# Kernel tuning notes

Hardware: AMD Instinct MI355X
Metric: run time of the kernel (lower is better)

## Reference

```python
import jax, jax.numpy as jnp
import numpy as np

L, B, T, H = 2, 512, 4096, 3


def _gru_layer(x, h0, Wih, Whh, bih, bhh):
    # x: [B,T,H], h0: [B,H], Wih/Whh: [3H,H], bih/bhh: [3H]
    gi = jnp.einsum('bth,gh->btg', x, Wih) + bih  # [B,T,3H] input projections

    def step(h, gi_t):
        gh = h @ Whh.T + bhh                      # [B,3H]
        i_r, i_z, i_n = jnp.split(gi_t, 3, axis=-1)
        h_r, h_z, h_n = jnp.split(gh, 3, axis=-1)
        r = jax.nn.sigmoid(i_r + h_r)
        z = jax.nn.sigmoid(i_z + h_z)
        n = jnp.tanh(i_n + r * h_n)
        h_new = (1.0 - z) * n + z * h
        return h_new, h_new

    h_last, ys = jax.lax.scan(step, h0, jnp.swapaxes(gi, 0, 1))  # ys: [T,B,H]
    return jnp.swapaxes(ys, 0, 1), h_last


def setup_inputs() -> dict:
    key = jax.random.key(0)
    ks = jax.random.split(key, 7)
    s = 0.3  # roughly torch's uniform(-1/sqrt(H), 1/sqrt(H)) scale
    return {
        'x': jax.random.normal(ks[0], (B, T, H), jnp.float32),
        'h': jnp.zeros((L, B, H), jnp.float32),
        'W_ih': jax.random.normal(ks[1], (L, 3 * H, H), jnp.float32) * s,
        'W_hh': jax.random.normal(ks[2], (L, 3 * H, H), jnp.float32) * s,
        'b_ih': jax.random.normal(ks[3], (L, 3 * H), jnp.float32) * s,
        'b_hh': jax.random.normal(ks[4], (L, 3 * H), jnp.float32) * s,
        'W_dec': jax.random.normal(ks[5], (1, H), jnp.float32) * s,
        'b_dec': jax.random.normal(ks[6], (1,), jnp.float32) * s,
    }


def reference(x, h, W_ih, W_hh, b_ih, b_hh, W_dec, b_dec):
    hs = []
    out = x
    for l in range(L):  # small fixed layer count
        out, h_l = _gru_layer(out, h[l], W_ih[l], W_hh[l], b_ih[l], b_hh[l])
        hs.append(h_l)
    h_out = jnp.stack(hs, axis=0)          # [L,B,H]
    y = out @ W_dec.T + b_dec              # [B,T,1]
    return (y, h_out)
```

## Files before the change

kernel.cpp:

```cpp
#include <hip/hip_runtime.h>


constexpr int T = 4096;
constexpr int B = 512;
constexpr float LOG2E = 1.44269504088896340736f;

typedef float v2f __attribute__((ext_vector_type(2)));

__device__ __forceinline__ float fexp2(float v) { return __builtin_amdgcn_exp2f(v); }
__device__ __forceinline__ float frcp(float v)  { return __builtin_amdgcn_rcpf(v); }
__device__ __forceinline__ v2f vfma(v2f a, v2f b, v2f c) {
    return __builtin_elementwise_fma(a, b, c);
}
__device__ __forceinline__ v2f sp(float x) { v2f r; r.x = x; r.y = x; return r; }

template<int CTRL>
__device__ __forceinline__ float dppf(float v) {
    return __int_as_float(
        __builtin_amdgcn_update_dpp(0, __float_as_int(v), CTRL, 0xF, 0xF, true));
}

#define GRU_IT(MODE, X0, X1, X2, YV) do {                                      \
    float hb0 = dppf<0x00>(h), hb1 = dppf<0x55>(h), hb2 = dppf<0xAA>(h);       \
    float s0 = dppf<0x114>(hb0), s1 = dppf<0x114>(hb1), s2 = dppf<0x114>(hb2); \
    float in0 = is_q0 ? (X0) : s0;                                             \
    float in1 = is_q0 ? (X1) : s1;                                             \
    float in2 = is_q0 ? (X2) : s2;                                             \
    v2f arz = vfma(wirz0, sp(in0), brz);                  \
    arz = vfma(wirz1, sp(in1), arz);                                           \
    arz = vfma(wirz2, sp(in2), arz);                                           \
    v2f hrz = vfma(whrz1, sp(hb1), whrz0 * sp(hb0));      \
    hrz = vfma(whrz2, sp(hb2), hrz);                                           \
    v2f crz = arz + hrz;                                                       \
    float r  = frcp(1.0f + fexp2(crz.x));                                      \
    float zz = frcp(1.0f + fexp2(crz.y));                                      \
    v2f cnd = vfma(wnd1, sp(hb1), vfma(wnd0, sp(hb0), bnd));    \
    cnd = vfma(wnd2, sp(hb2), cnd);                                            \
    YV = cnd.y;                                                                \
    float gi = fmaf(win1, in1, fmaf(win0, in0, bni));                          \
    gi = fmaf(win2, in2, gi);                                                  \
    float nn = fmaf(-2.0f, frcp(1.0f + fexp2(fmaf(r, cnd.x, gi))), 1.0f);      \
    float omz = 1.0f - zz;                                                     \
    float zh  = zz * h;                                                        \
    float hn  = fmaf(omz, nn, zh);                          \
    if ((MODE) == 0)      h = hn;                                              \
    else if ((MODE) == 1) h = is_q0 ? hn : h;                                  \
    else                  h = is_q0 ? h : hn;                                  \
} while (0)

__global__ __launch_bounds__(64, 1)
void gru_pipe(const float* __restrict__ x,
              const float* __restrict__ h0,
              const float* __restrict__ Wih,
              const float* __restrict__ Whh,
              const float* __restrict__ bih,
              const float* __restrict__ bhh,
              const float* __restrict__ Wdec,
              const float* __restrict__ bdec,
              float* __restrict__ out)
{
    const int lane  = threadIdx.x;
    const int g8    = lane & 7;
    const int layer = (g8 >> 2) & 1;
    const int jj    = g8 & 3;
    const int j     = jj > 2 ? 2 : jj;
    const bool dummy = (jj == 3);
    const bool is_q0 = (layer == 0);
    const int b = (blockIdx.x * 64 + lane) >> 3;

    const float zm = dummy ? 0.0f : 1.0f;
    const float sR = -LOG2E * zm, sN = 2.0f * LOG2E * zm;
    const float* Wi = Wih + layer * 27;
    const float* Wh = Whh + layer * 27;
    const float* bi = bih + layer * 9;
    const float* bh = bhh + layer * 9;

    v2f wirz0, wirz1, wirz2, whrz0, whrz1, whrz2, brz;
    wirz0.x = Wi[j*3+0]*sR;     wirz0.y = Wi[(3+j)*3+0]*sR;
    wirz1.x = Wi[j*3+1]*sR;     wirz1.y = Wi[(3+j)*3+1]*sR;
    wirz2.x = Wi[j*3+2]*sR;     wirz2.y = Wi[(3+j)*3+2]*sR;
    whrz0.x = Wh[j*3+0]*sR;     whrz0.y = Wh[(3+j)*3+0]*sR;
    whrz1.x = Wh[j*3+1]*sR;     whrz1.y = Wh[(3+j)*3+1]*sR;
    whrz2.x = Wh[j*3+2]*sR;     whrz2.y = Wh[(3+j)*3+2]*sR;
    brz.x   = (bi[j] + bh[j]) * sR;
    brz.y   = (bi[3+j] + bh[3+j]) * sR;

    const float wd0 = Wdec[0], wd1 = Wdec[1], wd2 = Wdec[2], bd = bdec[0];
    v2f wnd0, wnd1, wnd2, bnd;
    wnd0.x = Wh[(6+j)*3+0]*sN;  wnd0.y = wd0;
    wnd1.x = Wh[(6+j)*3+1]*sN;  wnd1.y = wd1;
    wnd2.x = Wh[(6+j)*3+2]*sN;  wnd2.y = wd2;
    bnd.x  = bh[6+j]*sN;        bnd.y  = bd;

    const float win0 = Wi[(6+j)*3+0]*sN, win1 = Wi[(6+j)*3+1]*sN,
                win2 = Wi[(6+j)*3+2]*sN;
    const float bni  = bi[6+j]*sN;

    float h = dummy ? 0.0f : h0[layer * B * 3 + b * 3 + j];

    const float4* xb = reinterpret_cast<const float4*>(x + (size_t)b * T * 3);
    float* yo = out + (size_t)b * T;

    float4 nx0 = xb[0], nx1 = xb[1], nx2 = xb[2];
    float4 cu0 = xb[3], cu1 = xb[4], cu2 = xb[5];
    float y0, y1, y2, y3, p2, p3;

    {
        GRU_IT(1, nx0.x, nx0.y, nx0.z, y0);
        GRU_IT(0, nx0.w, nx1.x, nx1.y, y1);
        GRU_IT(0, nx1.z, nx1.w, nx2.x, y2);
        GRU_IT(0, nx2.y, nx2.z, nx2.w, y3);
        p2 = y2; p3 = y3;
    }
    nx0 = xb[6]; nx1 = xb[7]; nx2 = xb[8];

    #pragma unroll 1
    for (int tc = 1; tc <= 1021; tc += 2) {
        const float4* pfa = xb + (tc + 2) * 3;
        float4 La0 = pfa[0], La1 = pfa[1], La2 = pfa[2];
        GRU_IT(0, cu0.x, cu0.y, cu0.z, y0);
        GRU_IT(0, cu0.w, cu1.x, cu1.y, y1);
        GRU_IT(0, cu1.z, cu1.w, cu2.x, y2);
        GRU_IT(0, cu2.y, cu2.z, cu2.w, y3);
        if (g8 == 7) {
            float4 q; q.x = p2; q.y = p3; q.z = y0; q.w = y1;
            *(float4*)(yo + 4 * tc - 4) = q;
        }
        p2 = y2; p3 = y3;
        const float4* pfb = xb + (((tc + 3) & 1023) * 3);
        float4 Lb0 = pfb[0], Lb1 = pfb[1], Lb2 = pfb[2];
        GRU_IT(0, nx0.x, nx0.y, nx0.z, y0);
        GRU_IT(0, nx0.w, nx1.x, nx1.y, y1);
        GRU_IT(0, nx1.z, nx1.w, nx2.x, y2);
        GRU_IT(0, nx2.y, nx2.z, nx2.w, y3);
        if (g8 == 7) {
            float4 q; q.x = p2; q.y = p3; q.z = y0; q.w = y1;
            *(float4*)(yo + 4 * tc) = q;
        }
        p2 = y2; p3 = y3;
        cu0 = La0; cu1 = La1; cu2 = La2;
        nx0 = Lb0; nx1 = Lb1; nx2 = Lb2;
    }

    GRU_IT(0, cu0.x, cu0.y, cu0.z, y0);
    GRU_IT(0, cu0.w, cu1.x, cu1.y, y1);
    GRU_IT(0, cu1.z, cu1.w, cu2.x, y2);
    GRU_IT(0, cu2.y, cu2.z, cu2.w, y3);
    if (g8 == 7) {
        float4 q; q.x = p2; q.y = p3; q.z = y0; q.w = y1;
        *(float4*)(yo + 4088) = q;
    }
    p2 = y2; p3 = y3;

    GRU_IT(2, 0.0f, 0.0f, 0.0f, y0);
    {
        float hb0 = dppf<0x00>(h), hb1 = dppf<0x55>(h), hb2 = dppf<0xAA>(h);
        y1 = fmaf(wd2, hb2, fmaf(wd1, hb1, fmaf(wd0, hb0, bd)));
    }
    if (g8 == 7) {
        float4 q; q.x = p2; q.y = p3; q.z = y0; q.w = y1;
        *(float4*)(yo + 4092) = q;
    }

    if (!dummy) out[B * T + (layer * B + b) * 3 + j] = h;
}

extern "C" void kernel_launch(void* const* d_in, const int* in_sizes, int n_in,
                              void* d_out, int out_size, void* d_ws, size_t ws_size,
                              hipStream_t stream) {
    const float* x    = (const float*)d_in[0];
    const float* h0   = (const float*)d_in[1];
    const float* Wih  = (const float*)d_in[2];
    const float* Whh  = (const float*)d_in[3];
    const float* bih  = (const float*)d_in[4];
    const float* bhh  = (const float*)d_in[5];
    const float* Wdec = (const float*)d_in[6];
    const float* bdec = (const float*)d_in[7];
    float* out = (float*)d_out;

    gru_pipe<<<(B * 8) / 64, 64, 0, stream>>>(x, h0, Wih, Whh, bih, bhh,
                                              Wdec, bdec, out);
}
```

Baseline: 481.6 us.

## Fuse layer-input select into DPP and merge sigmoid/tanh reciprocals in GRU step

Replaces the three row-shift DPPs plus per-lane selects with a single masked DPP (bank mask 0xA, no bound_ctrl) that keeps x in layer-0 lanes and pulls the previous-layer hidden state in layer-1 lanes. The gate update is rewritten algebraically so that the z-sigmoid and the tanh share one reciprocal: h' = (h*(F+1) + Ez*(F-1)) / ((F+1)(1+Ez)). Packed v2f FMAs are dropped in favour of scalar FMAs. The goal is a shorter per-step dependency chain and fewer transcendental ops. The risk is more scalar VALU instructions, and the product in the denominator can overflow for large exponents.

```diff
diff --git a/kernel.cpp b/kernel.cpp
--- a/kernel.cpp
+++ b/kernel.cpp
@@ -5,14 +5,8 @@
 constexpr int B = 512;
 constexpr float LOG2E = 1.44269504088896340736f;
 
-typedef float v2f __attribute__((ext_vector_type(2)));
-
 __device__ __forceinline__ float fexp2(float v) { return __builtin_amdgcn_exp2f(v); }
 __device__ __forceinline__ float frcp(float v)  { return __builtin_amdgcn_rcpf(v); }
-__device__ __forceinline__ v2f vfma(v2f a, v2f b, v2f c) {
-    return __builtin_elementwise_fma(a, b, c);
-}
-__device__ __forceinline__ v2f sp(float x) { v2f r; r.x = x; r.y = x; return r; }
 
 template<int CTRL>
 __device__ __forceinline__ float dppf(float v) {
@@ -20,29 +14,35 @@
         __builtin_amdgcn_update_dpp(0, __float_as_int(v), CTRL, 0xF, 0xF, true));
 }
 
+__device__ __forceinline__ float dpp_sel(float xv, float hbv) {
+    return __int_as_float(__builtin_amdgcn_update_dpp(
+        __float_as_int(xv), __float_as_int(hbv), 0x114, 0xF, 0xA, false));
+}
+
 #define GRU_IT(MODE, X0, X1, X2, YV) do {                                      \
     float hb0 = dppf<0x00>(h), hb1 = dppf<0x55>(h), hb2 = dppf<0xAA>(h);       \
-    float s0 = dppf<0x114>(hb0), s1 = dppf<0x114>(hb1), s2 = dppf<0x114>(hb2); \
-    float in0 = is_q0 ? (X0) : s0;                                             \
-    float in1 = is_q0 ? (X1) : s1;                                             \
-    float in2 = is_q0 ? (X2) : s2;                                             \
-    v2f arz = vfma(wirz0, sp(in0), brz);                  \
-    arz = vfma(wirz1, sp(in1), arz);                                           \
-    arz = vfma(wirz2, sp(in2), arz);                                           \
-    v2f hrz = vfma(whrz1, sp(hb1), whrz0 * sp(hb0));      \
-    hrz = vfma(whrz2, sp(hb2), hrz);                                           \
-    v2f crz = arz + hrz;                                                       \
-    float r  = frcp(1.0f + fexp2(crz.x));                                      \
-    float zz = frcp(1.0f + fexp2(crz.y));                                      \
-    v2f cnd = vfma(wnd1, sp(hb1), vfma(wnd0, sp(hb0), bnd));    \
-    cnd = vfma(wnd2, sp(hb2), cnd);                                            \
-    YV = cnd.y;                                                                \
-    float gi = fmaf(win1, in1, fmaf(win0, in0, bni));                          \
-    gi = fmaf(win2, in2, gi);                                                  \
-    float nn = fmaf(-2.0f, frcp(1.0f + fexp2(fmaf(r, cnd.x, gi))), 1.0f);      \
-    float omz = 1.0f - zz;                                                     \
-    float zh  = zz * h;                                                        \
-    float hn  = fmaf(omz, nn, zh);                          \
+    float in0 = dpp_sel((X0), hb0);                                            \
+    float in1 = dpp_sel((X1), hb1);                                            \
+    float in2 = dpp_sel((X2), hb2);                                            \
+    YV = fmaf(wd2, hb2, fmaf(wd1, hb1, fmaf(wd0, hb0, bd)));                   \
+    float crx = fmaf(wir2, in2, fmaf(wir1, in1, fmaf(wir0, in0, br)));         \
+    float crh = fmaf(whr2, hb2, fmaf(whr1, hb1, whr0 * hb0));                  \
+    float cr  = crx + crh;                                                     \
+    float czx = fmaf(wiz2, in2, fmaf(wiz1, in1, fmaf(wiz0, in0, bz)));         \
+    float czh = fmaf(whz2, hb2, fmaf(whz1, hb1, whz0 * hb0));                  \
+    float cz  = czx + czh;                                                     \
+    float gh  = fmaf(whn2, hb2, fmaf(whn1, hb1, fmaf(whn0, hb0, bnh)));        \
+    float gi  = fmaf(win2, in2, fmaf(win1, in1, fmaf(win0, in0, bni)));        \
+    float Er  = fexp2(cr);                                                     \
+    float rr  = frcp(1.0f + Er);                                               \
+    float aa  = fmaf(rr, gh, gi);                                              \
+    float F   = fexp2(aa);                                                     \
+    float Ez  = fexp2(cz);                                                     \
+    float Fp  = F + 1.0f;                                                      \
+    float Fm  = F - 1.0f;                                                      \
+    float Ezp = Ez + 1.0f;                                                     \
+    float num = fmaf(h, Fp, Ez * Fm);                  \
+    float hn  = num * frcp(Fp * Ezp);                                          \
     if ((MODE) == 0)      h = hn;                                              \
     else if ((MODE) == 1) h = is_q0 ? hn : h;                                  \
     else                  h = is_q0 ? h : hn;                                  \
@@ -75,26 +75,17 @@
     const float* bi = bih + layer * 9;
     const float* bh = bhh + layer * 9;
 
-    v2f wirz0, wirz1, wirz2, whrz0, whrz1, whrz2, brz;
-    wirz0.x = Wi[j*3+0]*sR;     wirz0.y = Wi[(3+j)*3+0]*sR;
-    wirz1.x = Wi[j*3+1]*sR;     wirz1.y = Wi[(3+j)*3+1]*sR;
-    wirz2.x = Wi[j*3+2]*sR;     wirz2.y = Wi[(3+j)*3+2]*sR;
-    whrz0.x = Wh[j*3+0]*sR;     whrz0.y = Wh[(3+j)*3+0]*sR;
-    whrz1.x = Wh[j*3+1]*sR;     whrz1.y = Wh[(3+j)*3+1]*sR;
-    whrz2.x = Wh[j*3+2]*sR;     whrz2.y = Wh[(3+j)*3+2]*sR;
-    brz.x   = (bi[j] + bh[j]) * sR;
-    brz.y   = (bi[3+j] + bh[3+j]) * sR;
-
+    const float wir0 = Wi[j*3+0]*sR, wir1 = Wi[j*3+1]*sR, wir2 = Wi[j*3+2]*sR;
+    const float wiz0 = Wi[(3+j)*3+0]*sR, wiz1 = Wi[(3+j)*3+1]*sR, wiz2 = Wi[(3+j)*3+2]*sR;
+    const float win0 = Wi[(6+j)*3+0]*sN, win1 = Wi[(6+j)*3+1]*sN, win2 = Wi[(6+j)*3+2]*sN;
+    const float whr0 = Wh[j*3+0]*sR, whr1 = Wh[j*3+1]*sR, whr2 = Wh[j*3+2]*sR;
+    const float whz0 = Wh[(3+j)*3+0]*sR, whz1 = Wh[(3+j)*3+1]*sR, whz2 = Wh[(3+j)*3+2]*sR;
+    const float whn0 = Wh[(6+j)*3+0]*sN, whn1 = Wh[(6+j)*3+1]*sN, whn2 = Wh[(6+j)*3+2]*sN;
+    const float br  = (bi[j] + bh[j]) * sR;
+    const float bz  = (bi[3+j] + bh[3+j]) * sR;
+    const float bni = bi[6+j] * sN;
+    const float bnh = bh[6+j] * sN;
     const float wd0 = Wdec[0], wd1 = Wdec[1], wd2 = Wdec[2], bd = bdec[0];
-    v2f wnd0, wnd1, wnd2, bnd;
-    wnd0.x = Wh[(6+j)*3+0]*sN;  wnd0.y = wd0;
-    wnd1.x = Wh[(6+j)*3+1]*sN;  wnd1.y = wd1;
-    wnd2.x = Wh[(6+j)*3+2]*sN;  wnd2.y = wd2;
-    bnd.x  = bh[6+j]*sN;        bnd.y  = bd;
-
-    const float win0 = Wi[(6+j)*3+0]*sN, win1 = Wi[(6+j)*3+1]*sN,
-                win2 = Wi[(6+j)*3+2]*sN;
-    const float bni  = bi[6+j]*sN;
 
     float h = dummy ? 0.0f : h0[layer * B * 3 + b * 3 + j];
 
```

Result: no change. 484.4 us (+0.6%).
